# Kernel optimization log

Measured on AMD Instinct MI355X. Metric: run time of the kernel, lower is better.

## Reference

```python
import jax, jax.numpy as jnp
import numpy as np
from functools import partial

ITERS = 100
EPSILON = 0.8
TAU = 1.02
FEATURE_DIM = 256
MATCHED_THRESHOLD = 0.2
B, D, N0, N1 = 1, 256, 2048, 2048


def log_optimal_transport_extended(scores, alpha, iters, epsilon, tau):
    b, m, n = scores.shape
    dt = scores.dtype
    ms = jnp.asarray(m, dt)
    ns = jnp.asarray(n, dt)
    bins0 = jnp.broadcast_to(alpha, (b, m, 1)).astype(dt)
    bins1 = jnp.broadcast_to(alpha, (b, 1, n)).astype(dt)
    corner = jnp.broadcast_to(alpha, (b, 1, 1)).astype(dt)
    # couplings: [b, m+1, n+1] score matrix augmented with dustbin row/col
    couplings = jnp.concatenate([
        jnp.concatenate([scores, bins0], axis=-1),
        jnp.concatenate([bins1, corner], axis=-1)], axis=1)
    norm = -jnp.log(ms + ns)
    log_mu = jnp.concatenate([jnp.full((m,), norm, dt), (jnp.log(ns) + norm)[None]])
    log_nu = jnp.concatenate([jnp.full((n,), norm, dt), (jnp.log(ms) + norm)[None]])
    log_mu = jnp.broadcast_to(log_mu[None], (b, m + 1))
    log_nu = jnp.broadcast_to(log_nu[None], (b, n + 1))

    def step(carry, _):
        u, v = carry
        u_new = (log_mu - jax.scipy.special.logsumexp(couplings + v[:, None, :], axis=2)) / tau
        u = u + epsilon * (u_new - u)
        v_new = (log_nu - jax.scipy.special.logsumexp(couplings + u[:, :, None], axis=1)) / tau
        v = v + epsilon * (v_new - v)
        return (u, v), None

    u0 = jnp.zeros_like(log_mu)
    v0 = jnp.zeros_like(log_nu)
    (u, v), _ = jax.lax.scan(jax.checkpoint(step), (u0, v0), None, length=iters)
    Z = couplings + u[:, :, None] + v[:, None, :]
    return Z - norm


def reference(mdesc0, mdesc1, bin_score):
    # mdesc0: [b, d, n], mdesc1: [b, d, m]
    sim = jnp.einsum('bdn,bdm->bnm', mdesc0, mdesc1)
    scores = sim / np.float32(np.sqrt(FEATURE_DIM))
    Z = log_optimal_transport_extended(scores, bin_score, ITERS, EPSILON, TAU)
    inner = Z[:, :-1, :-1]                       # [b, m, n]
    m, n = inner.shape[1], inner.shape[2]
    max0_vals = inner.max(axis=2)
    indices0 = inner.argmax(axis=2)              # [b, m] int
    indices1 = inner.argmax(axis=1)              # [b, n] int
    mutual0 = jnp.arange(m)[None, :] == jnp.take_along_axis(indices1, indices0, axis=1)
    mutual1 = jnp.arange(n)[None, :] == jnp.take_along_axis(indices0, indices1, axis=1)
    zero = jnp.zeros((), inner.dtype)
    mscores0 = jnp.where(mutual0, jnp.exp(max0_vals), zero)
    mscores1 = jnp.where(mutual1, jnp.take_along_axis(mscores0, indices1, axis=1), zero)
    valid0 = mutual0 & (mscores0 > MATCHED_THRESHOLD)
    valid1 = mutual1 & jnp.take_along_axis(valid0, indices1, axis=1)
    i0 = jnp.where(valid0, indices0, -1)
    i1 = jnp.where(valid1, indices1, -1)
    return (jnp.exp(Z[0]), i0[0], i1[0], mscores0[0], mscores1[0])


def setup_inputs() -> dict:
    key = jax.random.key(0)
    k0, k1 = jax.random.split(key)
    mdesc0 = jax.random.normal(k0, (B, D, N0), dtype=jnp.float32)
    mdesc1 = jax.random.normal(k1, (B, D, N1), dtype=jnp.float32)
    bin_score = jnp.ones((), dtype=jnp.float32)  # learned dustbin score, init 1.0
    return {"mdesc0": mdesc0, "mdesc1": mdesc1, "bin_score": bin_score}
```

## Files before the change

### kernel.cpp

```cpp
#include <hip/hip_runtime.h>
#include <hip/hip_bf16.h>
#include <math.h>

#define D        256
#define NINNER   2048
#define NROW     2049
#define SP       2064
#define ITERS_N  100
#define EPS_F    0.8f
#define TAU_F    1.02f
#define NB       256
#define NT       256

typedef unsigned long long u64;

#define PSTRIDE  2112u

#define SZ_MAT   (2049u * 2064u)
#define OFF_E    0u
#define OFF_F    SZ_MAT
#define OFF_WUP  (2u * SZ_MAT)
#define OFF_WVP  (OFF_WUP + 4u * PSTRIDE)
#define OFF_MAX0 (OFF_WVP + 4u * PSTRIDE)
#define OFF_IDX0 (OFF_MAX0 + 2048u)
#define OFF_IDX1 (OFF_IDX0 + 2048u)
#define OFF_MS0  (OFF_IDX1 + 2048u)
#define OFF_VLD0 (OFF_MS0 + 2048u)

#define OOFF_Z   0u
#define OOFF_I0  (2049u * 2049u)
#define OOFF_I1  (OOFF_I0 + 2048u)
#define OOFF_S0  (OOFF_I1 + 2048u)
#define OOFF_S1  (OOFF_S0 + 2048u)

__device__ __forceinline__ float    pair_val(u64 x) { return __uint_as_float((unsigned)x); }
__device__ __forceinline__ unsigned pair_tag(u64 x) { return (unsigned)(x >> 32); }
__device__ __forceinline__ u64 make_pair(float v, unsigned t) {
    return ((u64)t << 32) | (u64)__float_as_uint(v);
}

__global__ __launch_bounds__(256) void k_gemm(const float* __restrict__ A,
                                              const float* __restrict__ Bm,
                                              float* __restrict__ E,
                                              float* __restrict__ F) {
    __shared__ float As[8][64];
    __shared__ float Bs[8][64];
    const int tid = threadIdx.x;
    const int tx = tid & 15, ty = tid >> 4;
    const int row0 = blockIdx.y * 64, col0 = blockIdx.x * 64;
    float acc[4][4] = {};
    const int lr = tid >> 6, lc = tid & 63;
    for (int k0 = 0; k0 < D; k0 += 8) {
        As[lr][lc]     = A[(k0 + lr) * NINNER + row0 + lc];
        As[lr + 4][lc] = A[(k0 + lr + 4) * NINNER + row0 + lc];
        Bs[lr][lc]     = Bm[(k0 + lr) * NINNER + col0 + lc];
        Bs[lr + 4][lc] = Bm[(k0 + lr + 4) * NINNER + col0 + lc];
        __syncthreads();
#pragma unroll
        for (int kk = 0; kk < 8; ++kk) {
            const float4 av = *(const float4*)&As[kk][ty * 4];
            const float4 bv = *(const float4*)&Bs[kk][tx * 4];
            const float a_[4] = {av.x, av.y, av.z, av.w};
            const float b_[4] = {bv.x, bv.y, bv.z, bv.w};
#pragma unroll
            for (int r = 0; r < 4; ++r)
#pragma unroll
                for (int c = 0; c < 4; ++c)
                    acc[r][c] = fmaf(a_[r], b_[c], acc[r][c]);
        }
        __syncthreads();
    }
    float o[4][4];
#pragma unroll
    for (int r = 0; r < 4; ++r)
#pragma unroll
        for (int c = 0; c < 4; ++c)
            o[r][c] = expf(acc[r][c] * 0.0625f);
    const int row = row0 + ty * 4, col = col0 + tx * 4;
#pragma unroll
    for (int r = 0; r < 4; ++r)
        *(float4*)(E + (size_t)(row + r) * SP + col)
            = make_float4(o[r][0], o[r][1], o[r][2], o[r][3]);
#pragma unroll
    for (int c = 0; c < 4; ++c)
        *(float4*)(F + (size_t)(col + c) * SP + row)
            = make_float4(o[0][c], o[1][c], o[2][c], o[3][c]);
}

__global__ __launch_bounds__(256) void k_init(float* __restrict__ E,
                                              float* __restrict__ F,
                                              u64* __restrict__ wvb0,
                                              const float* __restrict__ alpha) {
    const int t = blockIdx.x * 256 + threadIdx.x;
    const float ea = expf(alpha[0]);
    if (t < NINNER) {
        E[(size_t)t * SP + NINNER] = ea;
        F[(size_t)t * SP + NINNER] = ea;
        wvb0[t] = make_pair(1.0f, 0u);
    }
    if (t <= NINNER) {
        E[(size_t)NINNER * SP + t] = ea;
        F[(size_t)NINNER * SP + t] = ea;
    }
}

__device__ __forceinline__ void poll8(const u64* buf, int tid, unsigned want, float* w) {
    u64 a[8];
#pragma unroll
    for (int q = 0; q < 8; ++q)
        a[q] = __hip_atomic_load(buf + q * 256 + tid, __ATOMIC_RELAXED, __HIP_MEMORY_SCOPE_AGENT);
    for (;;) {
        unsigned miss = 0u;
#pragma unroll
        for (int q = 0; q < 8; ++q)
            miss |= (pair_tag(a[q]) != want) ? (1u << q) : 0u;
        if (!miss) break;
        __builtin_amdgcn_s_sleep(2);
#pragma unroll
        for (int q = 0; q < 8; ++q)
            if (miss & (1u << q))
                a[q] = __hip_atomic_load(buf + q * 256 + tid, __ATOMIC_RELAXED, __HIP_MEMORY_SCOPE_AGENT);
    }
#pragma unroll
    for (int q = 0; q < 8; ++q) w[q] = pair_val(a[q]);
}

__global__ __launch_bounds__(256, 1) void k_sinkhorn(const float* __restrict__ E,
                                                     const float* __restrict__ F,
                                                     u64* wub, u64* wvb,
                                                     const float* __restrict__ alpha) {
    const int b = blockIdx.x, tid = threadIdx.x;
    const int lane = tid & 63, wid = tid >> 6;
    const int base = b * 8;
    const bool lastb = (b == NB - 1);
    __shared__ float red[2][4][9];

    const float norm = -8.317766166719343f;
    const float logbin = 7.624618986159398f + norm;
    const float ea = expf(alpha[0]);

    float eR[8][8], fR[8][8];
#pragma unroll
    for (int r = 0; r < 8; ++r) {
        const float* rowE = E + (size_t)(base + r) * SP;
        const float* rowF = F + (size_t)(base + r) * SP;
#pragma unroll
        for (int q = 0; q < 8; ++q) {
            eR[r][q] = rowE[q * 256 + tid];
            fR[r][q] = rowF[q * 256 + tid];
        }
    }

    float u = 0.0f, v = 0.0f;
    float ub = 0.0f, vb = 0.0f;
    float eub = 1.0f, evb = 1.0f;

    for (int it = 0; it < ITERS_N; ++it) {
        {
            const u64* src = wvb + (size_t)(it & 1) * PSTRIDE;
            u64* dst = wub + (size_t)((it + 1) & 1) * PSTRIDE;
            const unsigned prod = (unsigned)(it + 1);
            float w[8];
            poll8(src, tid, (unsigned)it, w);
            float p[8];
#pragma unroll
            for (int r = 0; r < 8; ++r) {
                float s = 0.0f;
#pragma unroll
                for (int q = 0; q < 8; ++q) s = fmaf(eR[r][q], w[q], s);
                p[r] = s;
            }
            float t = w[0] + w[1] + w[2] + w[3] + w[4] + w[5] + w[6] + w[7];
#pragma unroll
            for (int r = 0; r < 8; ++r) {
                float s = p[r];
#pragma unroll
                for (int m = 1; m < 64; m <<= 1) s += __shfl_xor(s, m, 64);
                if (lane == 0) red[0][wid][r] = s;
            }
#pragma unroll
            for (int m = 1; m < 64; m <<= 1) t += __shfl_xor(t, m, 64);
            if (lane == 0) red[0][wid][8] = t;
            __syncthreads();
            const float tsum = red[0][0][8] + red[0][1][8] + red[0][2][8] + red[0][3][8];
            const float Sbin = ea * (tsum + evb);
            ub = ub + EPS_F * ((logbin - logf(Sbin)) / TAU_F - ub);
            if (tid < 8) {
                const float S = red[0][0][tid] + red[0][1][tid] + red[0][2][tid] + red[0][3][tid]
                              + ea * evb;
                const float unew = (norm - logf(S)) / TAU_F;
                u = u + EPS_F * (unew - u);
                __hip_atomic_store(dst + base + tid, make_pair(expf(u), prod),
                                   __ATOMIC_RELAXED, __HIP_MEMORY_SCOPE_AGENT);
            }
            eub = expf(ub);
        }
        {
            const u64* src = wub + (size_t)((it + 1) & 1) * PSTRIDE;
            u64* dst = wvb + (size_t)((it + 1) & 1) * PSTRIDE;
            const unsigned prod = (unsigned)(it + 1);
            float w[8];
            poll8(src, tid, prod, w);
            float p[8];
#pragma unroll
            for (int r = 0; r < 8; ++r) {
                float s = 0.0f;
#pragma unroll
                for (int q = 0; q < 8; ++q) s = fmaf(fR[r][q], w[q], s);
                p[r] = s;
            }
            float t = w[0] + w[1] + w[2] + w[3] + w[4] + w[5] + w[6] + w[7];
#pragma unroll
            for (int r = 0; r < 8; ++r) {
                float s = p[r];
#pragma unroll
                for (int m = 1; m < 64; m <<= 1) s += __shfl_xor(s, m, 64);
                if (lane == 0) red[1][wid][r] = s;
            }
#pragma unroll
            for (int m = 1; m < 64; m <<= 1) t += __shfl_xor(t, m, 64);
            if (lane == 0) red[1][wid][8] = t;
            __syncthreads();
            const float tsum = red[1][0][8] + red[1][1][8] + red[1][2][8] + red[1][3][8];
            const float Tbin = ea * (tsum + eub);
            vb = vb + EPS_F * ((logbin - logf(Tbin)) / TAU_F - vb);
            if (tid < 8) {
                const float T = red[1][0][tid] + red[1][1][tid] + red[1][2][tid] + red[1][3][tid]
                              + ea * eub;
                const float vnew = (norm - logf(T)) / TAU_F;
                v = v + EPS_F * (vnew - v);
                __hip_atomic_store(dst + base + tid, make_pair(expf(v), prod),
                                   __ATOMIC_RELAXED, __HIP_MEMORY_SCOPE_AGENT);
            }
            evb = expf(vb);
        }
    }
    if (lastb && tid == 0) {
        __hip_atomic_store(wub + NINNER, make_pair(eub, (unsigned)ITERS_N),
                           __ATOMIC_RELAXED, __HIP_MEMORY_SCOPE_AGENT);
        __hip_atomic_store(wvb + NINNER, make_pair(evb, (unsigned)ITERS_N),
                           __ATOMIC_RELAXED, __HIP_MEMORY_SCOPE_AGENT);
    }
}

__global__ __launch_bounds__(256) void k_finish(const float* __restrict__ E,
                                                const float* __restrict__ F,
                                                const float2* __restrict__ wup,
                                                const float2* __restrict__ wvp,
                                                float* __restrict__ out,
                                                float* __restrict__ max0,
                                                int* __restrict__ idx0,
                                                int* __restrict__ idx1) {
    const int i = blockIdx.x;
    const int tid = threadIdx.x;
    const int lane = tid & 63, wid = tid >> 6;
    __shared__ float sb[4]; __shared__ int si[4];

    {
        const float wui = wup[i].x * 4096.0f;
        const float* row = E + (size_t)i * SP;
        float best = -1.0f; int bidx = 0;
        for (int j = tid; j < NROW; j += 256) {
            const float val = row[j] * wvp[j].x * wui;
            out[(size_t)i * NROW + j] = val;
            if (j < NINNER && val > best) { best = val; bidx = j; }
        }
        if (i < NINNER) {
#pragma unroll
            for (int m = 1; m < 64; m <<= 1) {
                const float ob = __shfl_xor(best, m, 64);
                const int   oi = __shfl_xor(bidx, m, 64);
                if (ob > best || (ob == best && oi < bidx)) { best = ob; bidx = oi; }
            }
            if (lane == 0) { sb[wid] = best; si[wid] = bidx; }
            __syncthreads();
            if (tid == 0) {
                for (int k = 1; k < 4; ++k)
                    if (sb[k] > best || (sb[k] == best && si[k] < bidx)) { best = sb[k]; bidx = si[k]; }
                max0[i] = best; idx0[i] = bidx;
            }
        }
    }

    if (i < NINNER) {
        __syncthreads();
        const float* row = F + (size_t)i * SP;
        float best = -1.0f; int bidx = 0;
        for (int r = tid; r < NINNER; r += 256) {
            const float q = row[r] * wup[r].x;
            if (q > best) { best = q; bidx = r; }
        }
#pragma unroll
        for (int m = 1; m < 64; m <<= 1) {
            const float ob = __shfl_xor(best, m, 64);
            const int   oi = __shfl_xor(bidx, m, 64);
            if (ob > best || (ob == best && oi < bidx)) { best = ob; bidx = oi; }
        }
        if (lane == 0) { sb[wid] = best; si[wid] = bidx; }
        __syncthreads();
        if (tid == 0) {
            for (int k = 1; k < 4; ++k)
                if (sb[k] > best || (sb[k] == best && si[k] < bidx)) { best = sb[k]; bidx = si[k]; }
            idx1[i] = bidx;
        }
    }
}

__global__ __launch_bounds__(256) void k_match0(const float* __restrict__ max0,
                                                const int* __restrict__ idx0,
                                                const int* __restrict__ idx1,
                                                float* __restrict__ ms0,
                                                int* __restrict__ vld0,
                                                float* __restrict__ out) {
    const int i = blockIdx.x * 256 + threadIdx.x;
    if (i >= NINNER) return;
    const int j = idx0[i];
    const bool mut = (idx1[j] == i);
    const float ms = mut ? max0[i] : 0.0f;
    const bool val = mut && (ms > 0.2f);
    ms0[i] = ms; vld0[i] = val ? 1 : 0;
    out[OOFF_I0 + i] = val ? (float)j : -1.0f;
    out[OOFF_S0 + i] = ms;
}
__global__ __launch_bounds__(256) void k_match1(const int* __restrict__ idx0,
                                                const int* __restrict__ idx1,
                                                const float* __restrict__ ms0,
                                                const int* __restrict__ vld0,
                                                float* __restrict__ out) {
    const int j = blockIdx.x * 256 + threadIdx.x;
    if (j >= NINNER) return;
    const int i = idx1[j];
    const bool mut = (idx0[i] == j);
    const float ms = mut ? ms0[i] : 0.0f;
    const bool val = mut && (vld0[i] != 0);
    out[OOFF_I1 + j] = val ? (float)i : -1.0f;
    out[OOFF_S1 + j] = ms;
}

extern "C" void kernel_launch(void* const* d_in, const int* in_sizes, int n_in,
                              void* d_out, int out_size, void* d_ws, size_t ws_size,
                              hipStream_t stream) {
    const float* A     = (const float*)d_in[0];
    const float* Bm    = (const float*)d_in[1];
    const float* alpha = (const float*)d_in[2];

    float* ws = (float*)d_ws;
    float* E    = ws + OFF_E;
    float* F    = ws + OFF_F;
    u64*   wub  = (u64*)(ws + OFF_WUP);
    u64*   wvb  = (u64*)(ws + OFF_WVP);
    float* max0 = ws + OFF_MAX0;
    int*   idx0 = (int*)(ws + OFF_IDX0);
    int*   idx1 = (int*)(ws + OFF_IDX1);
    float* ms0  = ws + OFF_MS0;
    int*   vld0 = (int*)(ws + OFF_VLD0);
    float* out  = (float*)d_out;

    k_gemm<<<dim3(32, 32), 256, 0, stream>>>(A, Bm, E, F);
    k_init<<<dim3(16), 256, 0, stream>>>(E, F, wvb, alpha);
    k_sinkhorn<<<dim3(NB), NT, 0, stream>>>(E, F, wub, wvb, alpha);
    k_finish<<<dim3(NROW), 256, 0, stream>>>(E, F, (const float2*)wub, (const float2*)wvb,
                                             out, max0, idx0, idx1);
    k_match0<<<dim3(8), 256, 0, stream>>>(max0, idx0, idx1, ms0, vld0, out);
    k_match1<<<dim3(8), 256, 0, stream>>>(idx0, idx1, ms0, vld0, out);
}
```

Before: 899.7 us.

## Pack two scaling values per 64-bit flag word using sign-bit parity tags

The cross-block exchange buffers now carry two positive floats per 64-bit word, with the sign bits used as a phase tag in place of a 32-bit iteration counter. This halves the words each thread polls per half-iteration, from 8 to 4, and makes those reads contiguous per thread. The matrix register tiles are reloaded with a matching contiguous column mapping, and the bin-value log/exp update is moved after the publishing stores so it is off the critical path. The sleep in the spin loop is shortened. This relies on all scaling values being strictly positive and on a two-phase parity being enough to tell fresh data from stale across the double buffers.

After: 1.135 ms. +26.2%, slower.

```diff
diff --git a/kernel.cpp b/kernel.cpp
--- a/kernel.cpp
+++ b/kernel.cpp
@@ -14,7 +14,8 @@
 
 typedef unsigned long long u64;
 
-#define PSTRIDE  2112u
+#define PSTRIDE  1088u
+#define SGNMASK  0x8000000080000000ull
 
 #define SZ_MAT   (2049u * 2064u)
 #define OFF_E    0u
@@ -33,10 +34,9 @@
 #define OOFF_S0  (OOFF_I1 + 2048u)
 #define OOFF_S1  (OOFF_S0 + 2048u)
 
-__device__ __forceinline__ float    pair_val(u64 x) { return __uint_as_float((unsigned)x); }
-__device__ __forceinline__ unsigned pair_tag(u64 x) { return (unsigned)(x >> 32); }
-__device__ __forceinline__ u64 make_pair(float v, unsigned t) {
-    return ((u64)t << 32) | (u64)__float_as_uint(v);
+__device__ __forceinline__ u64 pack_pair(float lo, float hi, unsigned sbit31) {
+    return ((u64)(__float_as_uint(hi) | sbit31) << 32)
+         |  (u64)(__float_as_uint(lo) | sbit31);
 }
 
 __global__ __launch_bounds__(256) void k_gemm(const float* __restrict__ A,
@@ -89,40 +89,52 @@
 
 __global__ __launch_bounds__(256) void k_init(float* __restrict__ E,
                                               float* __restrict__ F,
-                                              u64* __restrict__ wvb0,
+                                              u64* __restrict__ wub,
+                                              u64* __restrict__ wvb,
                                               const float* __restrict__ alpha) {
     const int t = blockIdx.x * 256 + threadIdx.x;
     const float ea = expf(alpha[0]);
     if (t < NINNER) {
         E[(size_t)t * SP + NINNER] = ea;
         F[(size_t)t * SP + NINNER] = ea;
-        wvb0[t] = make_pair(1.0f, 0u);
     }
     if (t <= NINNER) {
         E[(size_t)NINNER * SP + t] = ea;
         F[(size_t)NINNER * SP + t] = ea;
     }
-}
-
-__device__ __forceinline__ void poll8(const u64* buf, int tid, unsigned want, float* w) {
-    u64 a[8];
-#pragma unroll
-    for (int q = 0; q < 8; ++q)
-        a[q] = __hip_atomic_load(buf + q * 256 + tid, __ATOMIC_RELAXED, __HIP_MEMORY_SCOPE_AGENT);
+    if (t < 1024) {
+        const u64 pos = pack_pair(1.0f, 1.0f, 0u);
+        const u64 neg = pack_pair(1.0f, 1.0f, 0x80000000u);
+        wvb[t]           = pos;
+        wvb[PSTRIDE + t] = neg;
+        wub[t]           = pos;
+        wub[PSTRIDE + t] = neg;
+    }
+}
+
+__device__ __forceinline__ void poll4(const u64* __restrict__ buf, int tid,
+                                      u64 expect, float* w) {
+    u64 a[4];
+#pragma unroll
+    for (int k = 0; k < 4; ++k)
+        a[k] = __hip_atomic_load(buf + 4 * tid + k, __ATOMIC_RELAXED, __HIP_MEMORY_SCOPE_AGENT);
     for (;;) {
         unsigned miss = 0u;
 #pragma unroll
-        for (int q = 0; q < 8; ++q)
-            miss |= (pair_tag(a[q]) != want) ? (1u << q) : 0u;
+        for (int k = 0; k < 4; ++k)
+            miss |= (((a[k] ^ expect) & SGNMASK) != 0ull) ? (1u << k) : 0u;
         if (!miss) break;
-        __builtin_amdgcn_s_sleep(2);
-#pragma unroll
-        for (int q = 0; q < 8; ++q)
-            if (miss & (1u << q))
-                a[q] = __hip_atomic_load(buf + q * 256 + tid, __ATOMIC_RELAXED, __HIP_MEMORY_SCOPE_AGENT);
-    }
-#pragma unroll
-    for (int q = 0; q < 8; ++q) w[q] = pair_val(a[q]);
+        __builtin_amdgcn_s_sleep(1);
+#pragma unroll
+        for (int k = 0; k < 4; ++k)
+            if (miss & (1u << k))
+                a[k] = __hip_atomic_load(buf + 4 * tid + k, __ATOMIC_RELAXED, __HIP_MEMORY_SCOPE_AGENT);
+    }
+#pragma unroll
+    for (int k = 0; k < 4; ++k) {
+        w[2 * k]     = fabsf(__uint_as_float((unsigned)a[k]));
+        w[2 * k + 1] = fabsf(__uint_as_float((unsigned)(a[k] >> 32)));
+    }
 }
 
 __global__ __launch_bounds__(256, 1) void k_sinkhorn(const float* __restrict__ E,
@@ -142,13 +154,14 @@
     float eR[8][8], fR[8][8];
 #pragma unroll
     for (int r = 0; r < 8; ++r) {
-        const float* rowE = E + (size_t)(base + r) * SP;
-        const float* rowF = F + (size_t)(base + r) * SP;
-#pragma unroll
-        for (int q = 0; q < 8; ++q) {
-            eR[r][q] = rowE[q * 256 + tid];
-            fR[r][q] = rowF[q * 256 + tid];
-        }
+        const float* rowE = E + (size_t)(base + r) * SP + 8 * tid;
+        const float* rowF = F + (size_t)(base + r) * SP + 8 * tid;
+        const float4 e0 = *(const float4*)rowE, e1 = *(const float4*)(rowE + 4);
+        const float4 f0 = *(const float4*)rowF, f1 = *(const float4*)(rowF + 4);
+        eR[r][0] = e0.x; eR[r][1] = e0.y; eR[r][2] = e0.z; eR[r][3] = e0.w;
+        eR[r][4] = e1.x; eR[r][5] = e1.y; eR[r][6] = e1.z; eR[r][7] = e1.w;
+        fR[r][0] = f0.x; fR[r][1] = f0.y; fR[r][2] = f0.z; fR[r][3] = f0.w;
+        fR[r][4] = f1.x; fR[r][5] = f1.y; fR[r][6] = f1.z; fR[r][7] = f1.w;
     }
 
     float u = 0.0f, v = 0.0f;
@@ -159,9 +172,10 @@
         {
             const u64* src = wvb + (size_t)(it & 1) * PSTRIDE;
             u64* dst = wub + (size_t)((it + 1) & 1) * PSTRIDE;
-            const unsigned prod = (unsigned)(it + 1);
+            const u64 expw = ((it >> 1) & 1) ? SGNMASK : 0ull;
+            const unsigned sbit = (((it + 1) >> 1) & 1) << 31;
             float w[8];
-            poll8(src, tid, (unsigned)it, w);
+            poll4(src, tid, expw, w);
             float p[8];
 #pragma unroll
             for (int r = 0; r < 8; ++r) {
@@ -182,25 +196,33 @@
             for (int m = 1; m < 64; m <<= 1) t += __shfl_xor(t, m, 64);
             if (lane == 0) red[0][wid][8] = t;
             __syncthreads();
-            const float tsum = red[0][0][8] + red[0][1][8] + red[0][2][8] + red[0][3][8];
-            const float Sbin = ea * (tsum + evb);
-            ub = ub + EPS_F * ((logbin - logf(Sbin)) / TAU_F - ub);
+            float eu = 0.0f;
             if (tid < 8) {
                 const float S = red[0][0][tid] + red[0][1][tid] + red[0][2][tid] + red[0][3][tid]
                               + ea * evb;
                 const float unew = (norm - logf(S)) / TAU_F;
                 u = u + EPS_F * (unew - u);
-                __hip_atomic_store(dst + base + tid, make_pair(expf(u), prod),
-                                   __ATOMIC_RELAXED, __HIP_MEMORY_SCOPE_AGENT);
-            }
+                eu = expf(u);
+            }
+            if (tid < 64) {
+                const float lo = __shfl(eu, 2 * tid, 64);
+                const float hi = __shfl(eu, 2 * tid + 1, 64);
+                if (tid < 4)
+                    __hip_atomic_store(dst + 4 * b + tid, pack_pair(lo, hi, sbit),
+                                       __ATOMIC_RELAXED, __HIP_MEMORY_SCOPE_AGENT);
+            }
+            const float tsum = red[0][0][8] + red[0][1][8] + red[0][2][8] + red[0][3][8];
+            const float Sbin = ea * (tsum + evb);
+            ub = ub + EPS_F * ((logbin - logf(Sbin)) / TAU_F - ub);
             eub = expf(ub);
         }
         {
             const u64* src = wub + (size_t)((it + 1) & 1) * PSTRIDE;
             u64* dst = wvb + (size_t)((it + 1) & 1) * PSTRIDE;
-            const unsigned prod = (unsigned)(it + 1);
+            const u64 expw = (((it + 1) >> 1) & 1) ? SGNMASK : 0ull;
+            const unsigned sbit = (((it + 1) >> 1) & 1) << 31;
             float w[8];
-            poll8(src, tid, prod, w);
+            poll4(src, tid, expw, w);
             float p[8];
 #pragma unroll
             for (int r = 0; r < 8; ++r) {
@@ -221,32 +243,37 @@
             for (int m = 1; m < 64; m <<= 1) t += __shfl_xor(t, m, 64);
             if (lane == 0) red[1][wid][8] = t;
             __syncthreads();
-            const float tsum = red[1][0][8] + red[1][1][8] + red[1][2][8] + red[1][3][8];
-            const float Tbin = ea * (tsum + eub);
-            vb = vb + EPS_F * ((logbin - logf(Tbin)) / TAU_F - vb);
+            float ev = 0.0f;
             if (tid < 8) {
                 const float T = red[1][0][tid] + red[1][1][tid] + red[1][2][tid] + red[1][3][tid]
                               + ea * eub;
                 const float vnew = (norm - logf(T)) / TAU_F;
                 v = v + EPS_F * (vnew - v);
-                __hip_atomic_store(dst + base + tid, make_pair(expf(v), prod),
-                                   __ATOMIC_RELAXED, __HIP_MEMORY_SCOPE_AGENT);
-            }
+                ev = expf(v);
+            }
+            if (tid < 64) {
+                const float lo = __shfl(ev, 2 * tid, 64);
+                const float hi = __shfl(ev, 2 * tid + 1, 64);
+                if (tid < 4)
+                    __hip_atomic_store(dst + 4 * b + tid, pack_pair(lo, hi, sbit),
+                                       __ATOMIC_RELAXED, __HIP_MEMORY_SCOPE_AGENT);
+            }
+            const float tsum = red[1][0][8] + red[1][1][8] + red[1][2][8] + red[1][3][8];
+            const float Tbin = ea * (tsum + eub);
+            vb = vb + EPS_F * ((logbin - logf(Tbin)) / TAU_F - vb);
             evb = expf(vb);
         }
     }
     if (lastb && tid == 0) {
-        __hip_atomic_store(wub + NINNER, make_pair(eub, (unsigned)ITERS_N),
-                           __ATOMIC_RELAXED, __HIP_MEMORY_SCOPE_AGENT);
-        __hip_atomic_store(wvb + NINNER, make_pair(evb, (unsigned)ITERS_N),
-                           __ATOMIC_RELAXED, __HIP_MEMORY_SCOPE_AGENT);
+        ((float*)wub)[2048] = eub;
+        ((float*)wvb)[2048] = evb;
     }
 }
 
 __global__ __launch_bounds__(256) void k_finish(const float* __restrict__ E,
                                                 const float* __restrict__ F,
-                                                const float2* __restrict__ wup,
-                                                const float2* __restrict__ wvp,
+                                                const float* __restrict__ wuf,
+                                                const float* __restrict__ wvf,
                                                 float* __restrict__ out,
                                                 float* __restrict__ max0,
                                                 int* __restrict__ idx0,
@@ -257,11 +284,11 @@
     __shared__ float sb[4]; __shared__ int si[4];
 
     {
-        const float wui = wup[i].x * 4096.0f;
+        const float wui = wuf[i] * 4096.0f;
         const float* row = E + (size_t)i * SP;
         float best = -1.0f; int bidx = 0;
         for (int j = tid; j < NROW; j += 256) {
-            const float val = row[j] * wvp[j].x * wui;
+            const float val = row[j] * wvf[j] * wui;
             out[(size_t)i * NROW + j] = val;
             if (j < NINNER && val > best) { best = val; bidx = j; }
         }
@@ -287,7 +314,7 @@
         const float* row = F + (size_t)i * SP;
         float best = -1.0f; int bidx = 0;
         for (int r = tid; r < NINNER; r += 256) {
-            const float q = row[r] * wup[r].x;
+            const float q = row[r] * wuf[r];
             if (q > best) { best = q; bidx = r; }
         }
 #pragma unroll
@@ -357,9 +384,9 @@
     float* out  = (float*)d_out;
 
     k_gemm<<<dim3(32, 32), 256, 0, stream>>>(A, Bm, E, F);
-    k_init<<<dim3(16), 256, 0, stream>>>(E, F, wvb, alpha);
+    k_init<<<dim3(9), 256, 0, stream>>>(E, F, wub, wvb, alpha);
     k_sinkhorn<<<dim3(NB), NT, 0, stream>>>(E, F, wub, wvb, alpha);
-    k_finish<<<dim3(NROW), 256, 0, stream>>>(E, F, (const float2*)wub, (const float2*)wvb,
+    k_finish<<<dim3(NROW), 256, 0, stream>>>(E, F, (const float*)wub, (const float*)wvb,
                                              out, max0, idx0, idx1);
     k_match0<<<dim3(8), 256, 0, stream>>>(max0, idx0, idx1, ms0, vld0, out);
     k_match1<<<dim3(8), 256, 0, stream>>>(idx0, idx1, ms0, vld0, out);
```

## Give each wave whole rows in Sinkhorn to drop block barrier and LDS reduction

Applied to the files above, without the earlier changes.

The persistent Sinkhorn kernel now has each wave own two full rows, with 32 columns per lane, instead of splitting each block's eight rows across all 256 threads. Each row's dot product finishes with a wave shuffle, which removes the shared-memory reduction and the per-phase __syncthreads. Polling is split into four chunks, so FMAs on chunks that have already arrived overlap with waiting on later ones. In exchange, every wave polls the whole 2048-entry vector, which is four times the atomic load traffic per block, and it needs more registers. The k_init grid is also shrunk to the number of blocks it actually needs.

Result: slower. 1.752 ms (+94.8%).

```diff
diff --git a/kernel.cpp b/kernel.cpp
--- a/kernel.cpp
+++ b/kernel.cpp
@@ -104,138 +104,133 @@
     }
 }
 
-__device__ __forceinline__ void poll8(const u64* buf, int tid, unsigned want, float* w) {
-    u64 a[8];
-#pragma unroll
-    for (int q = 0; q < 8; ++q)
-        a[q] = __hip_atomic_load(buf + q * 256 + tid, __ATOMIC_RELAXED, __HIP_MEMORY_SCOPE_AGENT);
-    for (;;) {
-        unsigned miss = 0u;
-#pragma unroll
-        for (int q = 0; q < 8; ++q)
-            miss |= (pair_tag(a[q]) != want) ? (1u << q) : 0u;
-        if (!miss) break;
-        __builtin_amdgcn_s_sleep(2);
-#pragma unroll
-        for (int q = 0; q < 8; ++q)
-            if (miss & (1u << q))
-                a[q] = __hip_atomic_load(buf + q * 256 + tid, __ATOMIC_RELAXED, __HIP_MEMORY_SCOPE_AGENT);
-    }
-#pragma unroll
-    for (int q = 0; q < 8; ++q) w[q] = pair_val(a[q]);
-}
-
 __global__ __launch_bounds__(256, 1) void k_sinkhorn(const float* __restrict__ E,
                                                      const float* __restrict__ F,
                                                      u64* wub, u64* wvb,
                                                      const float* __restrict__ alpha) {
     const int b = blockIdx.x, tid = threadIdx.x;
     const int lane = tid & 63, wid = tid >> 6;
-    const int base = b * 8;
-    const bool lastb = (b == NB - 1);
-    __shared__ float red[2][4][9];
-
+    const int row0 = b * 8 + 2 * wid;
     const float norm = -8.317766166719343f;
     const float logbin = 7.624618986159398f + norm;
     const float ea = expf(alpha[0]);
 
-    float eR[8][8], fR[8][8];
-#pragma unroll
-    for (int r = 0; r < 8; ++r) {
-        const float* rowE = E + (size_t)(base + r) * SP;
-        const float* rowF = F + (size_t)(base + r) * SP;
-#pragma unroll
-        for (int q = 0; q < 8; ++q) {
-            eR[r][q] = rowE[q * 256 + tid];
-            fR[r][q] = rowF[q * 256 + tid];
-        }
-    }
-
-    float u = 0.0f, v = 0.0f;
-    float ub = 0.0f, vb = 0.0f;
-    float eub = 1.0f, evb = 1.0f;
+    float eR[2][32], fR[2][32];
+#pragma unroll
+    for (int r = 0; r < 2; ++r) {
+        const float* rowE = E + (size_t)(row0 + r) * SP + lane;
+        const float* rowF = F + (size_t)(row0 + r) * SP + lane;
+#pragma unroll
+        for (int k = 0; k < 32; ++k) {
+            eR[r][k] = rowE[64 * k];
+            fR[r][k] = rowF[64 * k];
+        }
+    }
+
+    float u0 = 0.0f, u1 = 0.0f, v0 = 0.0f, v1 = 0.0f;
+    float ub = 0.0f, vb = 0.0f, eub = 1.0f, evb = 1.0f;
 
     for (int it = 0; it < ITERS_N; ++it) {
         {
             const u64* src = wvb + (size_t)(it & 1) * PSTRIDE;
             u64* dst = wub + (size_t)((it + 1) & 1) * PSTRIDE;
-            const unsigned prod = (unsigned)(it + 1);
-            float w[8];
-            poll8(src, tid, (unsigned)it, w);
-            float p[8];
-#pragma unroll
-            for (int r = 0; r < 8; ++r) {
-                float s = 0.0f;
-#pragma unroll
-                for (int q = 0; q < 8; ++q) s = fmaf(eR[r][q], w[q], s);
-                p[r] = s;
-            }
-            float t = w[0] + w[1] + w[2] + w[3] + w[4] + w[5] + w[6] + w[7];
-#pragma unroll
-            for (int r = 0; r < 8; ++r) {
-                float s = p[r];
-#pragma unroll
-                for (int m = 1; m < 64; m <<= 1) s += __shfl_xor(s, m, 64);
-                if (lane == 0) red[0][wid][r] = s;
-            }
-#pragma unroll
-            for (int m = 1; m < 64; m <<= 1) t += __shfl_xor(t, m, 64);
-            if (lane == 0) red[0][wid][8] = t;
-            __syncthreads();
-            const float tsum = red[0][0][8] + red[0][1][8] + red[0][2][8] + red[0][3][8];
-            const float Sbin = ea * (tsum + evb);
-            ub = ub + EPS_F * ((logbin - logf(Sbin)) / TAU_F - ub);
-            if (tid < 8) {
-                const float S = red[0][0][tid] + red[0][1][tid] + red[0][2][tid] + red[0][3][tid]
-                              + ea * evb;
-                const float unew = (norm - logf(S)) / TAU_F;
-                u = u + EPS_F * (unew - u);
-                __hip_atomic_store(dst + base + tid, make_pair(expf(u), prod),
+            const unsigned want = (unsigned)it, prod = (unsigned)(it + 1);
+            u64 a[32];
+#pragma unroll
+            for (int k = 0; k < 32; ++k)
+                a[k] = __hip_atomic_load(src + 64 * k + lane, __ATOMIC_RELAXED, __HIP_MEMORY_SCOPE_AGENT);
+            float p0 = 0.0f, p1 = 0.0f, ts = 0.0f;
+#pragma unroll
+            for (int c = 0; c < 4; ++c) {
+                for (;;) {
+                    unsigned miss = 0u;
+#pragma unroll
+                    for (int j = 0; j < 8; ++j)
+                        miss |= (pair_tag(a[8 * c + j]) != want) ? (1u << j) : 0u;
+                    if (!miss) break;
+                    __builtin_amdgcn_s_sleep(1);
+#pragma unroll
+                    for (int j = 0; j < 8; ++j)
+                        if (miss & (1u << j))
+                            a[8 * c + j] = __hip_atomic_load(src + 64 * (8 * c + j) + lane,
+                                                             __ATOMIC_RELAXED, __HIP_MEMORY_SCOPE_AGENT);
+                }
+#pragma unroll
+                for (int j = 0; j < 8; ++j) {
+                    const float wv = pair_val(a[8 * c + j]);
+                    p0 = fmaf(eR[0][8 * c + j], wv, p0);
+                    p1 = fmaf(eR[1][8 * c + j], wv, p1);
+                    ts += wv;
+                }
+            }
+#pragma unroll
+            for (int m = 1; m < 64; m <<= 1) {
+                p0 += __shfl_xor(p0, m, 64);
+                p1 += __shfl_xor(p1, m, 64);
+                ts += __shfl_xor(ts, m, 64);
+            }
+            const float S0 = p0 + ea * evb;
+            const float S1 = p1 + ea * evb;
+            u0 = u0 + EPS_F * ((norm - logf(S0)) / TAU_F - u0);
+            u1 = u1 + EPS_F * ((norm - logf(S1)) / TAU_F - u1);
+            const float eu0 = expf(u0), eu1 = expf(u1);
+            if (lane < 2)
+                __hip_atomic_store(dst + row0 + lane, make_pair(lane ? eu1 : eu0, prod),
                                    __ATOMIC_RELAXED, __HIP_MEMORY_SCOPE_AGENT);
-            }
+            ub = ub + EPS_F * ((logbin - logf(ea * (ts + evb))) / TAU_F - ub);
             eub = expf(ub);
         }
         {
             const u64* src = wub + (size_t)((it + 1) & 1) * PSTRIDE;
             u64* dst = wvb + (size_t)((it + 1) & 1) * PSTRIDE;
-            const unsigned prod = (unsigned)(it + 1);
-            float w[8];
-            poll8(src, tid, prod, w);
-            float p[8];
-#pragma unroll
-            for (int r = 0; r < 8; ++r) {
-                float s = 0.0f;
-#pragma unroll
-                for (int q = 0; q < 8; ++q) s = fmaf(fR[r][q], w[q], s);
-                p[r] = s;
-            }
-            float t = w[0] + w[1] + w[2] + w[3] + w[4] + w[5] + w[6] + w[7];
-#pragma unroll
-            for (int r = 0; r < 8; ++r) {
-                float s = p[r];
-#pragma unroll
-                for (int m = 1; m < 64; m <<= 1) s += __shfl_xor(s, m, 64);
-                if (lane == 0) red[1][wid][r] = s;
-            }
-#pragma unroll
-            for (int m = 1; m < 64; m <<= 1) t += __shfl_xor(t, m, 64);
-            if (lane == 0) red[1][wid][8] = t;
-            __syncthreads();
-            const float tsum = red[1][0][8] + red[1][1][8] + red[1][2][8] + red[1][3][8];
-            const float Tbin = ea * (tsum + eub);
-            vb = vb + EPS_F * ((logbin - logf(Tbin)) / TAU_F - vb);
-            if (tid < 8) {
-                const float T = red[1][0][tid] + red[1][1][tid] + red[1][2][tid] + red[1][3][tid]
-                              + ea * eub;
-                const float vnew = (norm - logf(T)) / TAU_F;
-                v = v + EPS_F * (vnew - v);
-                __hip_atomic_store(dst + base + tid, make_pair(expf(v), prod),
+            const unsigned want = (unsigned)(it + 1), prod = (unsigned)(it + 1);
+            u64 a[32];
+#pragma unroll
+            for (int k = 0; k < 32; ++k)
+                a[k] = __hip_atomic_load(src + 64 * k + lane, __ATOMIC_RELAXED, __HIP_MEMORY_SCOPE_AGENT);
+            float p0 = 0.0f, p1 = 0.0f, ts = 0.0f;
+#pragma unroll
+            for (int c = 0; c < 4; ++c) {
+                for (;;) {
+                    unsigned miss = 0u;
+#pragma unroll
+                    for (int j = 0; j < 8; ++j)
+                        miss |= (pair_tag(a[8 * c + j]) != want) ? (1u << j) : 0u;
+                    if (!miss) break;
+                    __builtin_amdgcn_s_sleep(1);
+#pragma unroll
+                    for (int j = 0; j < 8; ++j)
+                        if (miss & (1u << j))
+                            a[8 * c + j] = __hip_atomic_load(src + 64 * (8 * c + j) + lane,
+                                                             __ATOMIC_RELAXED, __HIP_MEMORY_SCOPE_AGENT);
+                }
+#pragma unroll
+                for (int j = 0; j < 8; ++j) {
+                    const float wu = pair_val(a[8 * c + j]);
+                    p0 = fmaf(fR[0][8 * c + j], wu, p0);
+                    p1 = fmaf(fR[1][8 * c + j], wu, p1);
+                    ts += wu;
+                }
+            }
+#pragma unroll
+            for (int m = 1; m < 64; m <<= 1) {
+                p0 += __shfl_xor(p0, m, 64);
+                p1 += __shfl_xor(p1, m, 64);
+                ts += __shfl_xor(ts, m, 64);
+            }
+            const float T0 = p0 + ea * eub;
+            const float T1 = p1 + ea * eub;
+            v0 = v0 + EPS_F * ((norm - logf(T0)) / TAU_F - v0);
+            v1 = v1 + EPS_F * ((norm - logf(T1)) / TAU_F - v1);
+            const float ev0 = expf(v0), ev1 = expf(v1);
+            if (lane < 2)
+                __hip_atomic_store(dst + row0 + lane, make_pair(lane ? ev1 : ev0, prod),
                                    __ATOMIC_RELAXED, __HIP_MEMORY_SCOPE_AGENT);
-            }
+            vb = vb + EPS_F * ((logbin - logf(ea * (ts + eub))) / TAU_F - vb);
             evb = expf(vb);
         }
     }
-    if (lastb && tid == 0) {
+    if (b == NB - 1 && tid == 0) {
         __hip_atomic_store(wub + NINNER, make_pair(eub, (unsigned)ITERS_N),
                            __ATOMIC_RELAXED, __HIP_MEMORY_SCOPE_AGENT);
         __hip_atomic_store(wvb + NINNER, make_pair(evb, (unsigned)ITERS_N),
@@ -357,7 +352,7 @@
     float* out  = (float*)d_out;
 
     k_gemm<<<dim3(32, 32), 256, 0, stream>>>(A, Bm, E, F);
-    k_init<<<dim3(16), 256, 0, stream>>>(E, F, wvb, alpha);
+    k_init<<<dim3(9), 256, 0, stream>>>(E, F, wvb, alpha);
     k_sinkhorn<<<dim3(NB), NT, 0, stream>>>(E, F, wub, wvb, alpha);
     k_finish<<<dim3(NROW), 256, 0, stream>>>(E, F, (const float2*)wub, (const float2*)wvb,
                                              out, max0, idx0, idx1);
```
